# Kernel optimization log

Hardware: AMD Instinct MI355X
Metric: run time of the kernel (lower is better)

The kernel has to match this reference:

```python
import jax, jax.numpy as jnp
import numpy as np

OUT = 7          # roi_align output size
SR = 2           # sampling_ratio
SCALE = 1.0 / 16.0
T_OUT = 16       # F.interpolate temporal target
EPS = 1e-6


def setup_inputs() -> dict:
    key = jax.random.key(0)
    ks = jax.random.split(key, 12)
    B, Cin, Cout, T, H, W = 1, 1536, 3072, 16, 14, 14
    y = jax.random.normal(ks[0], (B, Cin, T, H, W), jnp.float32)
    x_t = jax.random.normal(ks[1], (B, Cout, T, H, W), jnp.float32)
    # ROIs in 224x224 image coords (spatial_scale = 1/16): one [1,4] box per frame
    x1 = jax.random.uniform(ks[2], (T,), minval=0.0, maxval=112.0)
    y1 = jax.random.uniform(ks[3], (T,), minval=0.0, maxval=112.0)
    x2 = jnp.minimum(x1 + jax.random.uniform(ks[4], (T,), minval=80.0, maxval=112.0), 224.0)
    y2 = jnp.minimum(y1 + jax.random.uniform(ks[5], (T,), minval=80.0, maxval=112.0), 224.0)
    rois = jnp.stack([x1, y1, x2, y2], axis=-1)[:, None, :]  # [T,1,4]
    conv_w = jax.random.normal(ks[6], (Cout, Cin), jnp.float32) * 0.02
    conv_b = jax.random.normal(ks[7], (Cout,), jnp.float32) * 0.02
    gamma = 1.0 + 0.1 * jax.random.normal(ks[8], (Cout,), jnp.float32)
    beta = 0.1 * jax.random.normal(ks[9], (Cout,), jnp.float32)
    run_mean = 0.1 * jax.random.normal(ks[10], (Cout,), jnp.float32)
    run_var = jax.random.uniform(ks[11], (Cout,), minval=0.5, maxval=1.5)
    return dict(y=y, x_t=x_t, rois=rois, conv_w=conv_w, conv_b=conv_b,
                gamma=gamma, beta=beta, run_mean=run_mean, run_var=run_var)


def _bilinear_sample(img, ys, xs):
    # img: [C,H,W]; ys: [Sy]; xs: [Sx] -> [C,Sy,Sx]; torchvision roi_align semantics
    C, H, W = img.shape
    oy = (ys < -1.0) | (ys > H)
    ox = (xs < -1.0) | (xs > W)
    yc = jnp.clip(ys, 0.0, H - 1)
    xc = jnp.clip(xs, 0.0, W - 1)
    y0 = jnp.floor(yc).astype(jnp.int32)
    x0 = jnp.floor(xc).astype(jnp.int32)
    y1i = jnp.minimum(y0 + 1, H - 1)
    x1i = jnp.minimum(x0 + 1, W - 1)
    ly = yc - y0
    lx = xc - x0
    g = lambda yi, xi: img[:, yi[:, None], xi[None, :]]  # [C,Sy,Sx]
    wy0, wy1 = (1.0 - ly)[:, None], ly[:, None]
    wx0, wx1 = (1.0 - lx)[None, :], lx[None, :]
    val = (wy0 * wx0 * g(y0, x0) + wy0 * wx1 * g(y0, x1i)
           + wy1 * wx0 * g(y1i, x0) + wy1 * wx1 * g(y1i, x1i))
    mask = (~oy)[:, None] & (~ox)[None, :]
    return jnp.where(mask[None], val, 0.0)


def _roi_align(feat, boxes):
    # feat: [N,C,H,W]; boxes: [N,4] (one box per image, aligned=False, sampling_ratio=2)
    N, C, H, W = feat.shape
    b = boxes * SCALE
    bx1, by1, bx2, by2 = b[:, 0], b[:, 1], b[:, 2], b[:, 3]
    rw = jnp.maximum(bx2 - bx1, 1.0)
    rh = jnp.maximum(by2 - by1, 1.0)
    bw, bh = rw / OUT, rh / OUT
    # sample positions per bin: (bin + (i+0.5)/SR) * bin_size
    pos = (jnp.arange(OUT, dtype=jnp.float32)[:, None]
           + (jnp.arange(SR, dtype=jnp.float32)[None, :] + 0.5) / SR).reshape(-1)  # [OUT*SR]
    ys = by1[:, None] + pos[None, :] * bh[:, None]
    xs = bx1[:, None] + pos[None, :] * bw[:, None]
    vals = jax.vmap(_bilinear_sample)(feat, ys, xs)  # [N,C,OUT*SR,OUT*SR]
    return vals.reshape(N, C, OUT, SR, OUT, SR).mean(axis=(3, 5))


def reference(y, x_t, rois, conv_w, conv_b, gamma, beta, run_mean, run_var):
    B, Cout, T, Hf, Wf = x_t.shape
    # 1x1x1 Conv3d, stride (1,2,2)
    ys = y[:, :, :, ::2, ::2]                                   # [B,Cin,T,7,7]
    yp = jnp.einsum('bcthw,oc->bothw', ys, conv_w) + conv_b[None, :, None, None, None]
    # BatchNorm3d (eval, eps=1e-6) + GELU (exact)
    inv = gamma / jnp.sqrt(run_var + EPS)
    yp = (yp - run_mean[None, :, None, None, None]) * inv[None, :, None, None, None] \
         + beta[None, :, None, None, None]
    yp = jax.nn.gelu(yp, approximate=False)
    # nearest temporal interpolation to T_OUT (identity when Tin == 16)
    Tin = yp.shape[2]
    tidx = (jnp.arange(T_OUT) * Tin) // T_OUT
    yp = yp[:, :, tidx]                                          # [B,Cout,16,7,7]
    # fusion branch: roi_align over (B*T) frames
    ff = jnp.transpose(x_t, (0, 2, 1, 3, 4)).reshape(B * T, Cout, Hf, Wf)
    boxes = rois[:, 0, :]                                        # [T,4]
    mr = _roi_align(ff, boxes)                                   # [B*T,Cout,7,7]
    mr = jnp.transpose(mr.reshape(B, T, Cout, OUT, OUT), (0, 2, 1, 3, 4))
    weighted = yp * mr                                           # [B,Cout,16,7,7]
    # per-frame 7x7 scatter-write into zeros, same window logic as the torch loop
    bs = boxes * SCALE
    sxi = jnp.floor(bs[:, 0]).astype(jnp.int32)
    syi = jnp.floor(bs[:, 1]).astype(jnp.int32)
    exi = jnp.ceil(bs[:, 2]).astype(jnp.int32)
    eyi = jnp.ceil(bs[:, 3]).astype(jnp.int32)
    ml = jnp.where(sxi + 7 < 14, sxi, exi - 7)
    mt = jnp.where(syi + 7 < 14, syi, eyi - 7)
    def place(w_t, t_off, l_off):  # w_t: [B,Cout,7,7]
        z = jnp.zeros((B, Cout, Hf, Wf), w_t.dtype)
        return jax.lax.dynamic_update_slice(z, w_t, (0, 0, t_off, l_off))
    new_face = jax.vmap(place, in_axes=(2, 0, 0), out_axes=2)(weighted, mt, ml)
    return new_face + x_t
```

## Files before the change

kernel.cpp:

```cpp
#include <hip/hip_runtime.h>

#define KD 1536
#define ND 3072
#define MD 784
#define TT 16

typedef __attribute__((ext_vector_type(8))) short short8;
typedef __attribute__((ext_vector_type(4))) float floatx4;

__device__ __forceinline__ unsigned short f2bf(float f) {
    unsigned int x = __float_as_uint(f);
    unsigned int r = (x + 0x7fffu + ((x >> 16) & 1u)) >> 16;
    return (unsigned short)r;
}

__device__ __forceinline__ void gld_lds16(const unsigned short* g, unsigned short* l) {
    __builtin_amdgcn_global_load_lds((const __attribute__((address_space(1))) void*)g,
                                     (__attribute__((address_space(3))) void*)l, 16, 0, 0);
}

__global__ __launch_bounds__(256) void prep_k(const float* __restrict__ y,
                                              const float* __restrict__ x_t,
                                              const float* __restrict__ rois,
                                              const float* __restrict__ conv_w,
                                              unsigned short* __restrict__ Ap,
                                              unsigned short* __restrict__ Bp,
                                              float* __restrict__ mr) {
    __shared__ float sm[64 * 197];
    __shared__ float wx0s[14], wx1s[14], wy0s[14], wy1s[14];
    __shared__ int x0s[14], x1s[14], y0s[14], y1s[14], vxs[14], vys[14];
    const int bid = blockIdx.x;
    const int tid = threadIdx.x;

    const int t = bid / 48;
    const int o0 = (bid % 48) * 64;

    if (tid < 14) {
        float b0 = rois[t * 4 + 0] * 0.0625f, b1 = rois[t * 4 + 1] * 0.0625f;
        float b2 = rois[t * 4 + 2] * 0.0625f, b3 = rois[t * 4 + 3] * 0.0625f;
        float rw = fmaxf(b2 - b0, 1.0f), rh = fmaxf(b3 - b1, 1.0f);
        float bw = rw * (1.0f / 7.0f), bh = rh * (1.0f / 7.0f);
        int p = tid;
        float pos = (float)(p >> 1) + 0.25f + 0.5f * (float)(p & 1);
        float xs = b0 + pos * bw;
        float ysv = b1 + pos * bh;
        vxs[p] = (xs >= -1.0f && xs <= 14.0f);
        vys[p] = (ysv >= -1.0f && ysv <= 14.0f);
        float xc = fminf(fmaxf(xs, 0.0f), 13.0f);
        float yc = fminf(fmaxf(ysv, 0.0f), 13.0f);
        int x0 = (int)floorf(xc), y0 = (int)floorf(yc);
        x0s[p] = x0; y0s[p] = y0;
        x1s[p] = min(x0 + 1, 13); y1s[p] = min(y0 + 1, 13);
        float lx = xc - (float)x0, ly = yc - (float)y0;
        wx0s[p] = 1.0f - lx; wx1s[p] = lx; wy0s[p] = 1.0f - ly; wy1s[p] = ly;
    }
    for (int f = tid; f < 64 * 196; f += 256) {
        int c = f / 196, pix = f % 196;
        sm[c * 197 + pix] = x_t[(size_t)(o0 + c) * 3136 + t * 196 + pix];
    }
    __syncthreads();
    for (int item = tid; item < 64 * 49; item += 256) {
        int c = item & 63, ij = item >> 6;
        int i = ij / 7, j = ij % 7;
        const float* base = &sm[c * 197];
        float sum = 0.0f;
#pragma unroll
        for (int s = 0; s < 2; ++s) {
            int p = 2 * i + s;
#pragma unroll
            for (int u = 0; u < 2; ++u) {
                int q = 2 * j + u;
                if (vys[p] && vxs[q]) {
                    float v00 = base[y0s[p] * 14 + x0s[q]];
                    float v01 = base[y0s[p] * 14 + x1s[q]];
                    float v10 = base[y1s[p] * 14 + x0s[q]];
                    float v11 = base[y1s[p] * 14 + x1s[q]];
                    sum += wy0s[p] * (wx0s[q] * v00 + wx1s[q] * v01) +
                           wy1s[p] * (wx0s[q] * v10 + wx1s[q] * v11);
                }
            }
        }
        mr[(size_t)(t * 49 + ij) * ND + o0 + c] = 0.25f * sum;
    }

    if (bid < 384) {
        __syncthreads();
        int t2 = bid / 24, kc = bid % 24;
        for (int f = tid; f < 64 * 196; f += 256) {
            int c = f / 196, pix = f % 196;
            sm[c * 197 + pix] = y[(size_t)(kc * 64 + c) * 3136 + t2 * 196 + pix];
        }
        __syncthreads();
        for (int item = tid; item < 64 * 49; item += 256) {
            int c = item & 63, ij = item >> 6;
            int i = ij / 7, j = ij % 7;
            Ap[(size_t)(t2 * 49 + ij) * KD + kc * 64 + c] =
                f2bf(sm[c * 197 + (2 * i) * 14 + 2 * j]);
        }
    } else {
        size_t base = (size_t)(bid - 384) * 12288;
#pragma unroll
        for (int v = 0; v < 12; ++v) {
            size_t e = base + v * 1024 + tid * 4;
            float4 w4 = *(const float4*)(conv_w + e);
            ushort4 o;
            o.x = f2bf(w4.x); o.y = f2bf(w4.y); o.z = f2bf(w4.z); o.w = f2bf(w4.w);
            *(ushort4*)(Bp + e) = o;
        }
    }
}

__global__ __launch_bounds__(256, 4) void gemm_k(const unsigned short* __restrict__ Ap,
                                                 const unsigned short* __restrict__ Bp,
                                                 const float* __restrict__ cb,
                                                 const float* __restrict__ gm,
                                                 const float* __restrict__ bt,
                                                 const float* __restrict__ rm,
                                                 const float* __restrict__ rv,
                                                 float* __restrict__ mrW) {
    __shared__ unsigned short As[2][64 * 64];
    __shared__ unsigned short Bs[2][64 * 64];
    const int tid = threadIdx.x;
    const int n0 = blockIdx.x * 64;
    const int m0 = blockIdx.y * 64;
    const int wv = tid >> 6;
    const int lane = tid & 63;
    const int wm = wv >> 1, wn = wv & 1;
    const int l15 = lane & 15, quad = lane >> 4;
    const int prow = lane >> 3, pch = lane & 7;
    const int L = pch ^ (prow & 7);

    const unsigned short* gbase;
    unsigned short *lb0, *lb1;
    if (wv < 2) {
        gbase = Ap + (size_t)(m0 + wv * 32 + prow) * KD + L * 8;
        lb0 = &As[0][(wv * 32) * 64];
        lb1 = &As[1][(wv * 32) * 64];
    } else {
        gbase = Bp + (size_t)(n0 + (wv - 2) * 32 + prow) * KD + L * 8;
        lb0 = &Bs[0][((wv - 2) * 32) * 64];
        lb1 = &Bs[1][((wv - 2) * 32) * 64];
    }

    floatx4 acc00 = {0.f, 0.f, 0.f, 0.f}, acc01 = {0.f, 0.f, 0.f, 0.f};
    floatx4 acc10 = {0.f, 0.f, 0.f, 0.f}, acc11 = {0.f, 0.f, 0.f, 0.f};

#pragma unroll
    for (int j = 0; j < 4; ++j)
        gld_lds16(gbase + (size_t)j * 8 * KD, lb0 + j * 512);

    int p = 0;
    for (int kt = 0; kt < KD; kt += 64, p ^= 1) {
        __syncthreads();
        if (kt + 64 < KD) {
            unsigned short* lb = p ? lb0 : lb1;
            const unsigned short* gb = gbase + kt + 64;
#pragma unroll
            for (int j = 0; j < 4; ++j)
                gld_lds16(gb + (size_t)j * 8 * KD, lb + j * 512);
        }
        const unsigned short* Ab = &As[p][0];
        const unsigned short* Bb = &Bs[p][0];
#pragma unroll
        for (int ko = 0; ko < 2; ++ko) {
            int ch = ((ko * 4 + quad) ^ (l15 & 7)) * 8;
            short8 a0 = *(const short8*)(Ab + (wm * 32 + l15) * 64 + ch);
            short8 a1 = *(const short8*)(Ab + (wm * 32 + 16 + l15) * 64 + ch);
            short8 b0 = *(const short8*)(Bb + (wn * 32 + l15) * 64 + ch);
            short8 b1 = *(const short8*)(Bb + (wn * 32 + 16 + l15) * 64 + ch);
            acc00 = __builtin_amdgcn_mfma_f32_16x16x32_bf16(a0, b0, acc00, 0, 0, 0);
            acc01 = __builtin_amdgcn_mfma_f32_16x16x32_bf16(a0, b1, acc01, 0, 0, 0);
            acc10 = __builtin_amdgcn_mfma_f32_16x16x32_bf16(a1, b0, acc10, 0, 0, 0);
            acc11 = __builtin_amdgcn_mfma_f32_16x16x32_bf16(a1, b1, acc11, 0, 0, 0);
        }
    }

#pragma unroll
    for (int ni = 0; ni < 2; ++ni) {
        int n = n0 + wn * 32 + ni * 16 + l15;
        float scale = gm[n] / sqrtf(rv[n] + 1e-6f);
        float shift = (cb[n] - rm[n]) * scale + bt[n];
#pragma unroll
        for (int mi = 0; mi < 2; ++mi) {
            floatx4 a = (ni == 0) ? (mi == 0 ? acc00 : acc10) : (mi == 0 ? acc01 : acc11);
#pragma unroll
            for (int r = 0; r < 4; ++r) {
                int m = m0 + wm * 32 + mi * 16 + quad * 4 + r;
                if (m < MD) {
                    float v = a[r] * scale + shift;
                    float g = 0.5f * v * (1.0f + erff(v * 0.70710678118654752f));
                    size_t idx = (size_t)m * ND + n;
                    mrW[idx] = g * mrW[idx];
                }
            }
        }
    }
}

__global__ __launch_bounds__(256) void final_k(const float* __restrict__ x_t,
                                               const float* __restrict__ rois,
                                               const float* __restrict__ W,
                                               float* __restrict__ out) {
    __shared__ float Wl[49 * 65];
    const int o0 = blockIdx.x * 64;
    const int t = blockIdx.y;
    const int tid = threadIdx.x;

    float b0 = rois[t * 4 + 0] * 0.0625f, b1 = rois[t * 4 + 1] * 0.0625f;
    float b2 = rois[t * 4 + 2] * 0.0625f, b3 = rois[t * 4 + 3] * 0.0625f;
    int sxi = (int)floorf(b0), syi = (int)floorf(b1);
    int exi = (int)ceilf(b2), eyi = (int)ceilf(b3);
    int ml = (sxi + 7 < 14) ? sxi : exi - 7;
    int mt = (syi + 7 < 14) ? syi : eyi - 7;
    ml = min(max(ml, 0), 7);
    mt = min(max(mt, 0), 7);

    for (int idx = tid; idx < 49 * 64; idx += 256) {
        int c = idx & 63, ij = idx >> 6;
        Wl[ij * 65 + c] = W[(size_t)(t * 49 + ij) * ND + o0 + c];
    }
    __syncthreads();

    for (int i4 = tid; i4 < 3136; i4 += 256) {
        int c = i4 / 49, p4 = i4 % 49;
        size_t e0 = (size_t)(o0 + c) * 3136 + t * 196 + p4 * 4;
        float4 xv = *(const float4*)(x_t + e0);
        float r[4] = {xv.x, xv.y, xv.z, xv.w};
#pragma unroll
        for (int u = 0; u < 4; ++u) {
            int pix = p4 * 4 + u;
            int h = pix / 14, w = pix % 14;
            int i = h - mt, j = w - ml;
            if (i >= 0 && i < 7 && j >= 0 && j < 7)
                r[u] += Wl[(i * 7 + j) * 65 + c];
        }
        *(float4*)(out + e0) = make_float4(r[0], r[1], r[2], r[3]);
    }
}

extern "C" void kernel_launch(void* const* d_in, const int* in_sizes, int n_in,
                              void* d_out, int out_size, void* d_ws, size_t ws_size,
                              hipStream_t stream) {
    const float* y = (const float*)d_in[0];
    const float* x_t = (const float*)d_in[1];
    const float* rois = (const float*)d_in[2];
    const float* conv_w = (const float*)d_in[3];
    const float* cb = (const float*)d_in[4];
    const float* gm = (const float*)d_in[5];
    const float* bt = (const float*)d_in[6];
    const float* rm = (const float*)d_in[7];
    const float* rv = (const float*)d_in[8];
    float* out = (float*)d_out;

    char* ws = (char*)d_ws;
    unsigned short* Ap = (unsigned short*)ws;
    unsigned short* Bp = (unsigned short*)(ws + 2555904);
    float* mrW = (float*)(ws + 2555904 + 9437184);

    prep_k<<<768, 256, 0, stream>>>(y, x_t, rois, conv_w, Ap, Bp, mrW);
    gemm_k<<<dim3(ND / 64, 13), 256, 0, stream>>>(Ap, Bp, cb, gm, bt, rm, rv, mrW);
    final_k<<<dim3(ND / 64, TT), 256, 0, stream>>>(x_t, rois, mrW, out);
}
```

Before: 175.4 us.

## Fuse final scatter-add into GEMM epilogue with per-frame 64x128 tiles

```diff
diff --git a/kernel.cpp b/kernel.cpp
--- a/kernel.cpp
+++ b/kernel.cpp
@@ -110,101 +110,97 @@
     }
 }
 
-__global__ __launch_bounds__(256, 4) void gemm_k(const unsigned short* __restrict__ Ap,
+__global__ __launch_bounds__(256, 2) void gemm_k(const unsigned short* __restrict__ Ap,
                                                  const unsigned short* __restrict__ Bp,
                                                  const float* __restrict__ cb,
                                                  const float* __restrict__ gm,
                                                  const float* __restrict__ bt,
                                                  const float* __restrict__ rm,
                                                  const float* __restrict__ rv,
-                                                 float* __restrict__ mrW) {
-    __shared__ unsigned short As[2][64 * 64];
-    __shared__ unsigned short Bs[2][64 * 64];
+                                                 const float* __restrict__ mr,
+                                                 const float* __restrict__ x_t,
+                                                 const float* __restrict__ rois,
+                                                 float* __restrict__ out) {
+    __shared__ unsigned short smem[24576];
+    unsigned short* const As0 = smem;
+    unsigned short* const As1 = smem + 4096;
+    unsigned short* const Bs0 = smem + 8192;
+    unsigned short* const Bs1 = smem + 16384;
+
     const int tid = threadIdx.x;
-    const int n0 = blockIdx.x * 64;
-    const int m0 = blockIdx.y * 64;
+    const int n0 = blockIdx.x * 128;
+    const int t = blockIdx.y;
+    const int aRow0 = t * 49;
     const int wv = tid >> 6;
     const int lane = tid & 63;
     const int wm = wv >> 1, wn = wv & 1;
     const int l15 = lane & 15, quad = lane >> 4;
-    const int prow = lane >> 3, pch = lane & 7;
-    const int L = pch ^ (prow & 7);
-
-    const unsigned short* gbase;
-    unsigned short *lb0, *lb1;
-    if (wv < 2) {
-        gbase = Ap + (size_t)(m0 + wv * 32 + prow) * KD + L * 8;
-        lb0 = &As[0][(wv * 32) * 64];
-        lb1 = &As[1][(wv * 32) * 64];
-    } else {
-        gbase = Bp + (size_t)(n0 + (wv - 2) * 32 + prow) * KD + L * 8;
-        lb0 = &Bs[0][((wv - 2) * 32) * 64];
-        lb1 = &Bs[1][((wv - 2) * 32) * 64];
-    }
-
-    floatx4 acc00 = {0.f, 0.f, 0.f, 0.f}, acc01 = {0.f, 0.f, 0.f, 0.f};
-    floatx4 acc10 = {0.f, 0.f, 0.f, 0.f}, acc11 = {0.f, 0.f, 0.f, 0.f};
-
-#pragma unroll
-    for (int j = 0; j < 4; ++j)
-        gld_lds16(gbase + (size_t)j * 8 * KD, lb0 + j * 512);
-
+
+    floatx4 acc[2][4] = {};
+
+    auto stage = [&](unsigned short* aDst, unsigned short* bDst, int kt) {
+#pragma unroll
+        for (int v = 0; v < 2; ++v) {
+            int idx = wv * 128 + v * 64 + lane;
+            int row = idx >> 3, pch = idx & 7;
+            int L = pch ^ (row & 7);
+            gld_lds16(Ap + (size_t)(aRow0 + row) * KD + kt + L * 8,
+                      aDst + (wv * 128 + v * 64) * 8);
+        }
+#pragma unroll
+        for (int v = 0; v < 4; ++v) {
+            int idx = wv * 256 + v * 64 + lane;
+            int row = idx >> 3, pch = idx & 7;
+            int L = pch ^ (row & 7);
+            gld_lds16(Bp + (size_t)(n0 + row) * KD + kt + L * 8,
+                      bDst + (wv * 256 + v * 64) * 8);
+        }
+    };
+
+    stage(As0, Bs0, 0);
     int p = 0;
     for (int kt = 0; kt < KD; kt += 64, p ^= 1) {
         __syncthreads();
-        if (kt + 64 < KD) {
-            unsigned short* lb = p ? lb0 : lb1;
-            const unsigned short* gb = gbase + kt + 64;
-#pragma unroll
-            for (int j = 0; j < 4; ++j)
-                gld_lds16(gb + (size_t)j * 8 * KD, lb + j * 512);
-        }
-        const unsigned short* Ab = &As[p][0];
-        const unsigned short* Bb = &Bs[p][0];
+        if (kt + 64 < KD)
+            stage(p ? As0 : As1, p ? Bs0 : Bs1, kt + 64);
+        const unsigned short* Ab = p ? As1 : As0;
+        const unsigned short* Bb = p ? Bs1 : Bs0;
 #pragma unroll
         for (int ko = 0; ko < 2; ++ko) {
-            int ch = ((ko * 4 + quad) ^ (l15 & 7)) * 8;
+            const int ch = ((ko * 4 + quad) ^ (l15 & 7)) * 8;
             short8 a0 = *(const short8*)(Ab + (wm * 32 + l15) * 64 + ch);
             short8 a1 = *(const short8*)(Ab + (wm * 32 + 16 + l15) * 64 + ch);
-            short8 b0 = *(const short8*)(Bb + (wn * 32 + l15) * 64 + ch);
-            short8 b1 = *(const short8*)(Bb + (wn * 32 + 16 + l15) * 64 + ch);
-            acc00 = __builtin_amdgcn_mfma_f32_16x16x32_bf16(a0, b0, acc00, 0, 0, 0);
-            acc01 = __builtin_amdgcn_mfma_f32_16x16x32_bf16(a0, b1, acc01, 0, 0, 0);
-            acc10 = __builtin_amdgcn_mfma_f32_16x16x32_bf16(a1, b0, acc10, 0, 0, 0);
-            acc11 = __builtin_amdgcn_mfma_f32_16x16x32_bf16(a1, b1, acc11, 0, 0, 0);
-        }
-    }
-
-#pragma unroll
-    for (int ni = 0; ni < 2; ++ni) {
-        int n = n0 + wn * 32 + ni * 16 + l15;
+#pragma unroll
+            for (int ni = 0; ni < 4; ++ni) {
+                short8 bn = *(const short8*)(Bb + (wn * 64 + ni * 16 + l15) * 64 + ch);
+                acc[0][ni] = __builtin_amdgcn_mfma_f32_16x16x32_bf16(a0, bn, acc[0][ni], 0, 0, 0);
+                acc[1][ni] = __builtin_amdgcn_mfma_f32_16x16x32_bf16(a1, bn, acc[1][ni], 0, 0, 0);
+            }
+        }
+    }
+
+    __syncthreads();
+    float* Wl = (float*)smem;
+#pragma unroll
+    for (int ni = 0; ni < 4; ++ni) {
+        int cl = wn * 64 + ni * 16 + l15;
+        int n = n0 + cl;
         float scale = gm[n] / sqrtf(rv[n] + 1e-6f);
         float shift = (cb[n] - rm[n]) * scale + bt[n];
 #pragma unroll
         for (int mi = 0; mi < 2; ++mi) {
-            floatx4 a = (ni == 0) ? (mi == 0 ? acc00 : acc10) : (mi == 0 ? acc01 : acc11);
 #pragma unroll
             for (int r = 0; r < 4; ++r) {
-                int m = m0 + wm * 32 + mi * 16 + quad * 4 + r;
-                if (m < MD) {
-                    float v = a[r] * scale + shift;
+                int m = wm * 32 + mi * 16 + quad * 4 + r;
+                if (m < 49) {
+                    float v = acc[mi][ni][r] * scale + shift;
                     float g = 0.5f * v * (1.0f + erff(v * 0.70710678118654752f));
-                    size_t idx = (size_t)m * ND + n;
-                    mrW[idx] = g * mrW[idx];
+                    Wl[m * 132 + cl] = g * mr[(size_t)(aRow0 + m) * ND + n];
                 }
             }
         }
     }
-}
-
-__global__ __launch_bounds__(256) void final_k(const float* __restrict__ x_t,
-                                               const float* __restrict__ rois,
-                                               const float* __restrict__ W,
-                                               float* __restrict__ out) {
-    __shared__ float Wl[49 * 65];
-    const int o0 = blockIdx.x * 64;
-    const int t = blockIdx.y;
-    const int tid = threadIdx.x;
+    __syncthreads();
 
     float b0 = rois[t * 4 + 0] * 0.0625f, b1 = rois[t * 4 + 1] * 0.0625f;
     float b2 = rois[t * 4 + 2] * 0.0625f, b3 = rois[t * 4 + 3] * 0.0625f;
@@ -215,26 +211,20 @@
     ml = min(max(ml, 0), 7);
     mt = min(max(mt, 0), 7);
 
-    for (int idx = tid; idx < 49 * 64; idx += 256) {
-        int c = idx & 63, ij = idx >> 6;
-        Wl[ij * 65 + c] = W[(size_t)(t * 49 + ij) * ND + o0 + c];
-    }
-    __syncthreads();
-
-    for (int i4 = tid; i4 < 3136; i4 += 256) {
+    for (int i4 = tid; i4 < 128 * 49; i4 += 256) {
         int c = i4 / 49, p4 = i4 % 49;
-        size_t e0 = (size_t)(o0 + c) * 3136 + t * 196 + p4 * 4;
+        size_t e0 = (size_t)(n0 + c) * 3136 + t * 196 + p4 * 4;
         float4 xv = *(const float4*)(x_t + e0);
-        float r[4] = {xv.x, xv.y, xv.z, xv.w};
+        float r4[4] = {xv.x, xv.y, xv.z, xv.w};
 #pragma unroll
         for (int u = 0; u < 4; ++u) {
             int pix = p4 * 4 + u;
             int h = pix / 14, w = pix % 14;
             int i = h - mt, j = w - ml;
             if (i >= 0 && i < 7 && j >= 0 && j < 7)
-                r[u] += Wl[(i * 7 + j) * 65 + c];
-        }
-        *(float4*)(out + e0) = make_float4(r[0], r[1], r[2], r[3]);
+                r4[u] += Wl[(i * 7 + j) * 132 + c];
+        }
+        *(float4*)(out + e0) = make_float4(r4[0], r4[1], r4[2], r4[3]);
     }
 }
 
@@ -255,9 +245,8 @@
     char* ws = (char*)d_ws;
     unsigned short* Ap = (unsigned short*)ws;
     unsigned short* Bp = (unsigned short*)(ws + 2555904);
-    float* mrW = (float*)(ws + 2555904 + 9437184);
-
-    prep_k<<<768, 256, 0, stream>>>(y, x_t, rois, conv_w, Ap, Bp, mrW);
-    gemm_k<<<dim3(ND / 64, 13), 256, 0, stream>>>(Ap, Bp, cb, gm, bt, rm, rv, mrW);
-    final_k<<<dim3(ND / 64, TT), 256, 0, stream>>>(x_t, rois, mrW, out);
-}
+    float* mr = (float*)(ws + 2555904 + 9437184);
+
+    prep_k<<<768, 256, 0, stream>>>(y, x_t, rois, conv_w, Ap, Bp, mr);
+    gemm_k<<<dim3(ND / 128, TT), 256, 0, stream>>>(Ap, Bp, cb, gm, bt, rm, rv, mr, x_t, rois, out);
+}
```

After: 184.5 us. 5.2% more time.

## Fuse final scatter-add epilogue into GEMM with per-frame M tiling

Applied to the files above, without the earlier changes.

```diff
diff --git a/kernel.cpp b/kernel.cpp
--- a/kernel.cpp
+++ b/kernel.cpp
@@ -117,12 +117,20 @@
                                                  const float* __restrict__ bt,
                                                  const float* __restrict__ rm,
                                                  const float* __restrict__ rv,
-                                                 float* __restrict__ mrW) {
-    __shared__ unsigned short As[2][64 * 64];
-    __shared__ unsigned short Bs[2][64 * 64];
+                                                 const float* __restrict__ mr,
+                                                 const float* __restrict__ x_t,
+                                                 const float* __restrict__ rois,
+                                                 float* __restrict__ out) {
+    __shared__ unsigned short smem[16384];
+    unsigned short* const As0 = smem;
+    unsigned short* const As1 = smem + 4096;
+    unsigned short* const Bs0 = smem + 8192;
+    unsigned short* const Bs1 = smem + 12288;
+
     const int tid = threadIdx.x;
     const int n0 = blockIdx.x * 64;
-    const int m0 = blockIdx.y * 64;
+    const int t = blockIdx.y;
+    const int aRow0 = t * 49;
     const int wv = tid >> 6;
     const int lane = tid & 63;
     const int wm = wv >> 1, wn = wv & 1;
@@ -133,13 +141,13 @@
     const unsigned short* gbase;
     unsigned short *lb0, *lb1;
     if (wv < 2) {
-        gbase = Ap + (size_t)(m0 + wv * 32 + prow) * KD + L * 8;
-        lb0 = &As[0][(wv * 32) * 64];
-        lb1 = &As[1][(wv * 32) * 64];
+        gbase = Ap + (size_t)(aRow0 + wv * 32 + prow) * KD + L * 8;
+        lb0 = &As0[(wv * 32) * 64];
+        lb1 = &As1[(wv * 32) * 64];
     } else {
         gbase = Bp + (size_t)(n0 + (wv - 2) * 32 + prow) * KD + L * 8;
-        lb0 = &Bs[0][((wv - 2) * 32) * 64];
-        lb1 = &Bs[1][((wv - 2) * 32) * 64];
+        lb0 = &Bs0[((wv - 2) * 32) * 64];
+        lb1 = &Bs1[((wv - 2) * 32) * 64];
     }
 
     floatx4 acc00 = {0.f, 0.f, 0.f, 0.f}, acc01 = {0.f, 0.f, 0.f, 0.f};
@@ -159,8 +167,8 @@
             for (int j = 0; j < 4; ++j)
                 gld_lds16(gb + (size_t)j * 8 * KD, lb + j * 512);
         }
-        const unsigned short* Ab = &As[p][0];
-        const unsigned short* Bb = &Bs[p][0];
+        const unsigned short* Ab = p ? As1 : As0;
+        const unsigned short* Bb = p ? Bs1 : Bs0;
 #pragma unroll
         for (int ko = 0; ko < 2; ++ko) {
             int ch = ((ko * 4 + quad) ^ (l15 & 7)) * 8;
@@ -175,9 +183,12 @@
         }
     }
 
+    __syncthreads();
+    float* Wl = (float*)smem;
 #pragma unroll
     for (int ni = 0; ni < 2; ++ni) {
-        int n = n0 + wn * 32 + ni * 16 + l15;
+        int cl = wn * 32 + ni * 16 + l15;
+        int n = n0 + cl;
         float scale = gm[n] / sqrtf(rv[n] + 1e-6f);
         float shift = (cb[n] - rm[n]) * scale + bt[n];
 #pragma unroll
@@ -185,26 +196,16 @@
             floatx4 a = (ni == 0) ? (mi == 0 ? acc00 : acc10) : (mi == 0 ? acc01 : acc11);
 #pragma unroll
             for (int r = 0; r < 4; ++r) {
-                int m = m0 + wm * 32 + mi * 16 + quad * 4 + r;
-                if (m < MD) {
+                int m = wm * 32 + mi * 16 + quad * 4 + r;
+                if (m < 49) {
                     float v = a[r] * scale + shift;
                     float g = 0.5f * v * (1.0f + erff(v * 0.70710678118654752f));
-                    size_t idx = (size_t)m * ND + n;
-                    mrW[idx] = g * mrW[idx];
+                    Wl[m * 65 + cl] = g * mr[(size_t)(aRow0 + m) * ND + n];
                 }
             }
         }
     }
-}
-
-__global__ __launch_bounds__(256) void final_k(const float* __restrict__ x_t,
-                                               const float* __restrict__ rois,
-                                               const float* __restrict__ W,
-                                               float* __restrict__ out) {
-    __shared__ float Wl[49 * 65];
-    const int o0 = blockIdx.x * 64;
-    const int t = blockIdx.y;
-    const int tid = threadIdx.x;
+    __syncthreads();
 
     float b0 = rois[t * 4 + 0] * 0.0625f, b1 = rois[t * 4 + 1] * 0.0625f;
     float b2 = rois[t * 4 + 2] * 0.0625f, b3 = rois[t * 4 + 3] * 0.0625f;
@@ -215,26 +216,20 @@
     ml = min(max(ml, 0), 7);
     mt = min(max(mt, 0), 7);
 
-    for (int idx = tid; idx < 49 * 64; idx += 256) {
-        int c = idx & 63, ij = idx >> 6;
-        Wl[ij * 65 + c] = W[(size_t)(t * 49 + ij) * ND + o0 + c];
-    }
-    __syncthreads();
-
-    for (int i4 = tid; i4 < 3136; i4 += 256) {
+    for (int i4 = tid; i4 < 64 * 49; i4 += 256) {
         int c = i4 / 49, p4 = i4 % 49;
-        size_t e0 = (size_t)(o0 + c) * 3136 + t * 196 + p4 * 4;
+        size_t e0 = (size_t)(n0 + c) * 3136 + t * 196 + p4 * 4;
         float4 xv = *(const float4*)(x_t + e0);
-        float r[4] = {xv.x, xv.y, xv.z, xv.w};
+        float r4[4] = {xv.x, xv.y, xv.z, xv.w};
 #pragma unroll
         for (int u = 0; u < 4; ++u) {
             int pix = p4 * 4 + u;
             int h = pix / 14, w = pix % 14;
             int i = h - mt, j = w - ml;
             if (i >= 0 && i < 7 && j >= 0 && j < 7)
-                r[u] += Wl[(i * 7 + j) * 65 + c];
-        }
-        *(float4*)(out + e0) = make_float4(r[0], r[1], r[2], r[3]);
+                r4[u] += Wl[(i * 7 + j) * 65 + c];
+        }
+        *(float4*)(out + e0) = make_float4(r4[0], r4[1], r4[2], r4[3]);
     }
 }
 
@@ -255,9 +250,8 @@
     char* ws = (char*)d_ws;
     unsigned short* Ap = (unsigned short*)ws;
     unsigned short* Bp = (unsigned short*)(ws + 2555904);
-    float* mrW = (float*)(ws + 2555904 + 9437184);
-
-    prep_k<<<768, 256, 0, stream>>>(y, x_t, rois, conv_w, Ap, Bp, mrW);
-    gemm_k<<<dim3(ND / 64, 13), 256, 0, stream>>>(Ap, Bp, cb, gm, bt, rm, rv, mrW);
-    final_k<<<dim3(ND / 64, TT), 256, 0, stream>>>(x_t, rois, mrW, out);
-}
+    float* mr = (float*)(ws + 2555904 + 9437184);
+
+    prep_k<<<768, 256, 0, stream>>>(y, x_t, rois, conv_w, Ap, Bp, mr);
+    gemm_k<<<dim3(ND / 64, TT), 256, 0, stream>>>(Ap, Bp, cb, gm, bt, rm, rv, mr, x_t, rois, out);
+}
```

Measured after the change: 170.1 us. 1.03x faster.
